# Kernel tuning notes

Hardware: AMD Instinct MI355X
Metric: run time of the kernel (lower is better)

## Reference

```python
import jax, jax.numpy as jnp
import numpy as np

N_NODES = 100000
NUM_REL = 2


def rgcn_conv(x, src, dst, etype, W, root, bias):
    """PyG-style RGCNConv: per-relation mean aggregation + root transform + bias.
    x: [N, in], W: [R, in, out], root: [in, out], bias: [out].
    """
    R = W.shape[0]
    N = x.shape[0]
    # Pre-transform nodes by every relation weight: [R, N, out]
    xr = jnp.einsum('ni,rio->rno', x, W)
    msgs = xr[etype, src]  # [E, out] gather per-edge, relation-typed
    seg_id = dst * R + etype  # combined (node, relation) segment id
    summed = jax.ops.segment_sum(msgs, seg_id, num_segments=N * R)
    cnt = jax.ops.segment_sum(jnp.ones(etype.shape, x.dtype), seg_id, num_segments=N * R)
    summed = summed.reshape(N, R, -1)
    cnt = cnt.reshape(N, R, 1)
    agg = (summed / jnp.maximum(cnt, 1.0)).sum(axis=1)  # sum over relations of per-relation means
    return agg + x @ root + bias


def setup_inputs() -> dict:
    key = jax.random.key(0)
    ks = jax.random.split(key, 9)
    d = 128
    E = 800000
    sc = 1.0 / np.sqrt(d)
    return {
        'x': jax.random.normal(ks[0], (N_NODES, d), jnp.float32),
        'edge_index_a': jax.random.randint(ks[1], (2, E), 0, N_NODES, jnp.int64),
        'edge_index_b': jax.random.randint(ks[2], (2, E), 0, N_NODES, jnp.int64),
        'W1': jax.random.normal(ks[3], (NUM_REL, d, d), jnp.float32) * sc,
        'root1': jax.random.normal(ks[4], (d, d), jnp.float32) * sc,
        'b1': jnp.zeros((d,), jnp.float32),
        'W2': jax.random.normal(ks[5], (NUM_REL, d, d), jnp.float32) * sc,
        'root2': jax.random.normal(ks[6], (d, d), jnp.float32) * sc,
        'b2': jnp.zeros((d,), jnp.float32),
    }


def reference(x, edge_index_a, edge_index_b, W1, root1, b1, W2, root2, b2):
    # Concatenate per-relation edge lists + build edge_type ids (a->0, b->1)
    edge_index = jnp.concatenate([edge_index_a, edge_index_b], axis=1)
    etype = jnp.concatenate([
        jnp.zeros((edge_index_a.shape[1],), jnp.int32),
        jnp.ones((edge_index_b.shape[1],), jnp.int32),
    ])
    src, dst = edge_index[0], edge_index[1]
    h = rgcn_conv(x, src, dst, etype, W1, root1, b1)
    h = jax.nn.relu(h)
    out = rgcn_conv(h, src, dst, etype, W2, root2, b2)
    return out
```

## Files before the change

kernel.cpp:

```cpp
#include <hip/hip_runtime.h>
#include <hip/hip_bf16.h>


typedef __attribute__((ext_vector_type(8))) short bf16x8;
typedef __attribute__((ext_vector_type(4))) float f32x4;
typedef unsigned short ushort_t;
typedef unsigned int uint_t;

#define BSHIFT 9
#define SEGB (1 << (BSHIFT + 1))
#define NBMAX 256
#define SLAB 16384
#define CH_PER_THREAD 8
#define CHUNK (256 * CH_PER_THREAD)

#define GBM 256
#define KCH 128
#define LDBE 136

#define ROWB 768
#define XOFF 512

__device__ __forceinline__ ushort_t f2b(float f) {
  union { float f; uint_t u; } v;
  v.f = f;
  uint_t u = v.u;
  return (ushort_t)((u + 0x7FFFu + ((u >> 16) & 1u)) >> 16);
}
__device__ __forceinline__ void dot2acc(float& a, uint_t pk, uint_t sel) {
  asm("v_dot2_f32_bf16 %0, %1, %2, %0" : "+v"(a) : "v"(pk), "v"(sel));
}

__global__ __launch_bounds__(256) void prep_bin(
    const int* __restrict__ ea, const int* __restrict__ eb, int E, int NB,
    int* __restrict__ cursor, uint_t* __restrict__ staging, int nchunk,
    const float* __restrict__ W1, const float* __restrict__ root1,
    const float* __restrict__ W2, const float* __restrict__ root2,
    ushort_t* __restrict__ Bt1, ushort_t* __restrict__ Bt2,
    const float* __restrict__ x, ushort_t* __restrict__ aggbuf1, int N) {
  __shared__ int h[NBMAX];
  __shared__ int bbase[NBMAX];
  __shared__ int lofs[NBMAX];
  __shared__ int sscan[256];
  __shared__ uint_t sval[CHUNK];
  __shared__ int sdst[CHUNK];
  int b = blockIdx.x;
  int t = threadIdx.x;

  if (b < nchunk) {
    for (int i = t; i < NB; i += 256) h[i] = 0;
    __syncthreads();
    int tbase = b * CHUNK + t;
    int total = 2 * E;
    uint_t val[CH_PER_THREAD];
    short bktv[CH_PER_THREAD];
#pragma unroll
    for (int j = 0; j < CH_PER_THREAD; ++j) {
      int i = tbase + j * 256;
      if (i < total) {
        int src, dst, rel;
        if (i < E) { src = ea[i];     dst = ea[E + i]; rel = 0; }
        else       { src = eb[i - E]; dst = eb[i];     rel = 1; }
        int seg = dst * 2 + rel;
        int bkt = seg >> (BSHIFT + 1);
        val[j] = ((uint_t)src << 10) | (uint_t)(seg & (SEGB - 1));
        bktv[j] = (short)bkt;
        atomicAdd(&h[bkt], 1);
      } else {
        bktv[j] = -1;
      }
    }
    __syncthreads();
    {
      int v = (t < NB) ? h[t] : 0;
      sscan[t] = v;
      __syncthreads();
      for (int off = 1; off < 256; off <<= 1) {
        int tmp = (t >= off) ? sscan[t - off] : 0;
        __syncthreads();
        sscan[t] += tmp;
        __syncthreads();
      }
      if (t < NB) {
        lofs[t] = sscan[t] - v;
        bbase[t] = v ? t * SLAB + atomicAdd(&cursor[t], v) : 0;
      }
    }
    __syncthreads();
    for (int i = t; i < NB; i += 256) h[i] = 0;
    __syncthreads();
#pragma unroll
    for (int j = 0; j < CH_PER_THREAD; ++j) {
      if (bktv[j] >= 0) {
        int bkt = bktv[j];
        int r = atomicAdd(&h[bkt], 1);
        int pos = lofs[bkt] + r;
        sval[pos] = val[j];
        sdst[pos] = bbase[bkt] + r;
      }
    }
    __syncthreads();
    int nrec = 2 * E - b * CHUNK;
    if (nrec > CHUNK) nrec = CHUNK;
    for (int i = t; i < nrec; i += 256)
      staging[sdst[i]] = sval[i];
  } else if (b < nchunk + 384) {
    int flat = (b - nchunk) * 256 + t;
    int which = flat >= 49152;
    int idx = flat - which * 49152;
    int c = idx / 384;
    int k = idx - c * 384;
    const float* W = which ? W2 : W1;
    const float* root = which ? root2 : root1;
    ushort_t* Bt = which ? Bt2 : Bt1;
    float v = (k < 256) ? W[(size_t)k * 128 + c] : root[(size_t)(k - 256) * 128 + c];
    Bt[(size_t)c * 384 + k] = f2b(v);
  } else {
    int idx = (b - nchunk - 384) * 256 + t;
    int n = idx >> 6, lane = idx & 63;
    if (n < N) {
      float2 v = *(const float2*)(x + (size_t)n * 128 + lane * 2);
      uint_t pk = (uint_t)f2b(v.x) | ((uint_t)f2b(v.y) << 16);
      *(uint_t*)(aggbuf1 + (size_t)n * 384 + 256 + lane * 2) = pk;
    }
  }
}

__global__ __launch_bounds__(1024) void bucket_build(
    const uint_t* __restrict__ staging, const int* __restrict__ cursor,
    int* __restrict__ csr, int* __restrict__ offs,
    int* __restrict__ ends, int nseg) {
  __shared__ int scnt[SEGB];
  __shared__ int sexcl[SEGB];
  __shared__ int sdata[SEGB];
  int b = blockIdx.x;
  int t = threadIdx.x;
  int base = b * SLAB;
  int ne = cursor[b];
  int seg0 = b << (BSHIFT + 1);

  scnt[t] = 0;
  __syncthreads();
  const uint_t* st = staging + base;
  for (int i = t; i < ne; i += 1024)
    atomicAdd(&scnt[st[i] & (SEGB - 1)], 1);
  __syncthreads();
  int c = scnt[t];
  sdata[t] = c;
  __syncthreads();
  for (int off = 1; off < 1024; off <<= 1) {
    int tmp = (t >= off) ? sdata[t - off] : 0;
    __syncthreads();
    sdata[t] += tmp;
    __syncthreads();
  }
  int excl = sdata[t] - c;
  sexcl[t] = excl;
  {
    int g = seg0 + t;
    if (g < nseg) { offs[g] = base + excl; ends[g] = base + excl + c; }
  }
  scnt[t] = 0;
  __syncthreads();
  for (int i = t; i < ne; i += 1024) {
    uint_t rec = st[i];
    int seg = (int)(rec & (SEGB - 1));
    int src = (int)(rec >> 10);
    int r = atomicAdd(&scnt[seg], 1);
    csr[base + sexcl[seg] + r] = src * ROWB + XOFF;
  }
}

__global__ __launch_bounds__(256) void agg_kernel(
    const char* __restrict__ xbc,
    const int* __restrict__ csr,
    const int* __restrict__ offs, const int* __restrict__ ends,
    ushort_t* __restrict__ agg, int nseg) {
  int wid = (blockIdx.x * blockDim.x + threadIdx.x) >> 6;
  if (wid >= nseg) return;
  int lane = threadIdx.x & 63;
  int q = lane >> 4;
  int t = lane & 15;
  int beg = offs[wid], end = ends[wid];
  const uint_t sel_lo = 0x00003F80u;
  const uint_t sel_hi = 0x3F800000u;

  float acc[8];
#pragma unroll
  for (int j = 0; j < 8; ++j) acc[j] = 0.f;

  const char* xt = xbc + t * 16;
  int e = beg + q;
  for (; e + 4 < end; e += 8) {
    int o0 = csr[e];
    int o1 = csr[e + 4];
    uint4 v0 = *(const uint4*)(xt + o0);
    uint4 v1 = *(const uint4*)(xt + o1);
    dot2acc(acc[0], v0.x, sel_lo); dot2acc(acc[1], v0.x, sel_hi);
    dot2acc(acc[2], v0.y, sel_lo); dot2acc(acc[3], v0.y, sel_hi);
    dot2acc(acc[4], v0.z, sel_lo); dot2acc(acc[5], v0.z, sel_hi);
    dot2acc(acc[6], v0.w, sel_lo); dot2acc(acc[7], v0.w, sel_hi);
    dot2acc(acc[0], v1.x, sel_lo); dot2acc(acc[1], v1.x, sel_hi);
    dot2acc(acc[2], v1.y, sel_lo); dot2acc(acc[3], v1.y, sel_hi);
    dot2acc(acc[4], v1.z, sel_lo); dot2acc(acc[5], v1.z, sel_hi);
    dot2acc(acc[6], v1.w, sel_lo); dot2acc(acc[7], v1.w, sel_hi);
  }
  if (e < end) {
    int o0 = csr[e];
    uint4 v0 = *(const uint4*)(xt + o0);
    dot2acc(acc[0], v0.x, sel_lo); dot2acc(acc[1], v0.x, sel_hi);
    dot2acc(acc[2], v0.y, sel_lo); dot2acc(acc[3], v0.y, sel_hi);
    dot2acc(acc[4], v0.z, sel_lo); dot2acc(acc[5], v0.z, sel_hi);
    dot2acc(acc[6], v0.w, sel_lo); dot2acc(acc[7], v0.w, sel_hi);
  }

#pragma unroll
  for (int j = 0; j < 8; ++j) {
    acc[j] += __shfl_xor(acc[j], 16);
    acc[j] += __shfl_xor(acc[j], 32);
  }

  int c = end - beg;
  float inv = 1.0f / (float)(c > 1 ? c : 1);
  if (q == 0) {
    uint4 o;
    o.x = (uint_t)f2b(acc[0] * inv) | ((uint_t)f2b(acc[1] * inv) << 16);
    o.y = (uint_t)f2b(acc[2] * inv) | ((uint_t)f2b(acc[3] * inv) << 16);
    o.z = (uint_t)f2b(acc[4] * inv) | ((uint_t)f2b(acc[5] * inv) << 16);
    o.w = (uint_t)f2b(acc[6] * inv) | ((uint_t)f2b(acc[7] * inv) << 16);
    int n = wid >> 1, r = wid & 1;
    *(uint4*)(agg + (size_t)n * 384 + r * 128 + t * 8) = o;
  }
}

__device__ __forceinline__ void do_mfma32(
    const char* bs, f32x4 (&acc)[4][8], const bf16x8 (&a)[4],
    int ks, int lrow, int kg) {
  bf16x8 b[8];
#pragma unroll
  for (int c = 0; c < 8; ++c)
    b[c] = *(const bf16x8*)(bs + (c * 16 + lrow) * (LDBE * 2) +
                            (ks * 4 + kg) * 16);
#pragma unroll
  for (int r = 0; r < 4; ++r)
#pragma unroll
    for (int c = 0; c < 8; ++c)
      acc[r][c] = __builtin_amdgcn_mfma_f32_16x16x32_bf16(a[r], b[c], acc[r][c], 0, 0, 0);
}

template <int MODE>
__global__ __launch_bounds__(256, 2) void mfma_gemm(
    const ushort_t* __restrict__ A,
    const ushort_t* __restrict__ Bt,
    const float* __restrict__ bias,
    float* __restrict__ outf,
    ushort_t* __restrict__ outb,
    int M) {
  __shared__ __align__(16) ushort_t Bs[2][128 * LDBE];
  const int tid = threadIdx.x;
  const int lane = tid & 63;
  const int wave = tid >> 6;
  const int lrow = lane & 15;
  const int kg = lane >> 4;
  const int rowbase = blockIdx.x * GBM + wave * 64;

  f32x4 acc[4][8];
#pragma unroll
  for (int r = 0; r < 4; ++r)
#pragma unroll
    for (int c = 0; c < 8; ++c) acc[r][c] = (f32x4){0.f, 0.f, 0.f, 0.f};

  uint4 stg[8];
#pragma unroll
  for (int j = 0; j < 8; ++j) {
    int flat = tid + j * 256;
    int col = flat >> 4;
    int q = flat & 15;
    stg[j] = *(const uint4*)(Bt + (size_t)col * 384 + q * 8);
  }
#pragma unroll
  for (int j = 0; j < 8; ++j) {
    int flat = tid + j * 256;
    int col = flat >> 4;
    int q = flat & 15;
    *(uint4*)((char*)&Bs[0][0] + col * (LDBE * 2) + q * 16) = stg[j];
  }
  __syncthreads();

  int cur = 0;
  for (int ch = 0; ch < 3; ++ch) {
    if (ch < 2) {
#pragma unroll
      for (int j = 0; j < 8; ++j) {
        int flat = tid + j * 256;
        int col = flat >> 4;
        int q = flat & 15;
        stg[j] = *(const uint4*)(Bt + (size_t)col * 384 + (ch + 1) * KCH + q * 8);
      }
    }
    const ushort_t* ab = A + (size_t)ch * KCH + kg * 8;
    const char* bsbase = (const char*)&Bs[0][0] + cur * (128 * LDBE * 2);
    bf16x8 aA[4], aB[4];
#pragma unroll
    for (int r = 0; r < 4; ++r)
      aA[r] = *(const bf16x8*)(ab + (size_t)(rowbase + r * 16 + lrow) * 384);
#pragma unroll
    for (int r = 0; r < 4; ++r)
      aB[r] = *(const bf16x8*)(ab + (size_t)(rowbase + r * 16 + lrow) * 384 + 32);
    do_mfma32(bsbase, acc, aA, 0, lrow, kg);
#pragma unroll
    for (int r = 0; r < 4; ++r)
      aA[r] = *(const bf16x8*)(ab + (size_t)(rowbase + r * 16 + lrow) * 384 + 64);
    do_mfma32(bsbase, acc, aB, 1, lrow, kg);
#pragma unroll
    for (int r = 0; r < 4; ++r)
      aB[r] = *(const bf16x8*)(ab + (size_t)(rowbase + r * 16 + lrow) * 384 + 96);
    do_mfma32(bsbase, acc, aA, 2, lrow, kg);
    do_mfma32(bsbase, acc, aB, 3, lrow, kg);
    if (ch < 2) {
#pragma unroll
      for (int j = 0; j < 8; ++j) {
        int flat = tid + j * 256;
        int col = flat >> 4;
        int q = flat & 15;
        *(uint4*)((char*)&Bs[0][0] + (cur ^ 1) * (128 * LDBE * 2) +
                  col * (LDBE * 2) + q * 16) = stg[j];
      }
      __syncthreads();
      cur ^= 1;
    }
  }

  if (MODE == 1) {
    __syncthreads();
    ushort_t* ws = (ushort_t*)&Bs[0][0] + wave * (64 * 128);
#pragma unroll
    for (int c = 0; c < 8; ++c) {
      int col = c * 16 + lrow;
      float bv = bias[col];
#pragma unroll
      for (int r = 0; r < 4; ++r)
#pragma unroll
        for (int j = 0; j < 4; ++j) {
          float v = fmaxf(acc[r][c][j] + bv, 0.f);
          ws[(r * 16 + kg * 4 + j) * 128 + col] = f2b(v);
        }
    }
    __syncthreads();
#pragma unroll
    for (int rr = 0; rr < 16; ++rr) {
      int lr = rr * 4 + (lane >> 4);
      int row = rowbase + lr;
      int tq = lane & 15;
      if (row < M) {
        uint4 v = *(const uint4*)(ws + lr * 128 + tq * 8);
        *(uint4*)(outb + (size_t)row * 384 + 256 + tq * 8) = v;
      }
    }
  } else {
#pragma unroll
    for (int c = 0; c < 8; ++c) {
      int col = c * 16 + lrow;
      float bv = bias[col];
#pragma unroll
      for (int r = 0; r < 4; ++r) {
        int r0 = rowbase + r * 16 + kg * 4;
#pragma unroll
        for (int j = 0; j < 4; ++j) {
          int row = r0 + j;
          if (row < M) {
            outf[(size_t)row * 128 + col] = acc[r][c][j] + bv;
          }
        }
      }
    }
  }
}

extern "C" void kernel_launch(void* const* d_in, const int* in_sizes, int n_in,
                              void* d_out, int out_size, void* d_ws, size_t ws_size,
                              hipStream_t stream) {
  const float* x     = (const float*)d_in[0];
  const int*   ea    = (const int*)d_in[1];
  const int*   eb    = (const int*)d_in[2];
  const float* W1    = (const float*)d_in[3];
  const float* root1 = (const float*)d_in[4];
  const float* b1    = (const float*)d_in[5];
  const float* W2    = (const float*)d_in[6];
  const float* root2 = (const float*)d_in[7];
  const float* b2    = (const float*)d_in[8];
  float* out = (float*)d_out;

  const int N = in_sizes[0] / 128;
  const int E = in_sizes[1] / 2;
  const int nseg = N * 2;
  const int Mblk = (N + GBM - 1) / GBM;
  const int Mpad = Mblk * GBM;
  const int NB = ((N - 1) >> BSHIFT) + 1;
  const int nchunk = (2 * E + CHUNK - 1) / CHUNK;
  const int XSB = (N * 64 + 255) / 256;

  char* p = (char*)d_ws;
  ushort_t* aggbuf1 = (ushort_t*)p;  p += (size_t)Mpad * 384 * sizeof(ushort_t);
  ushort_t* aggbuf2 = (ushort_t*)p;  p += (size_t)Mpad * 384 * sizeof(ushort_t);
  ushort_t* Bt1 = (ushort_t*)p;      p += (size_t)128 * 384 * sizeof(ushort_t);
  ushort_t* Bt2 = (ushort_t*)p;      p += (size_t)128 * 384 * sizeof(ushort_t);
  int* csr = (int*)p;                p += (size_t)NBMAX * SLAB * sizeof(int);
  int* offs = (int*)p;               p += (size_t)nseg * sizeof(int);
  int* ends = (int*)p;               p += (size_t)nseg * sizeof(int);
  int* cursor = (int*)p;             p += NBMAX * sizeof(int);
  uint_t* staging = (uint_t*)aggbuf2;

  hipMemsetAsync(cursor, 0, NBMAX * sizeof(int), stream);

  prep_bin<<<nchunk + 384 + XSB, 256, 0, stream>>>(
      ea, eb, E, NB, cursor, staging, nchunk,
      W1, root1, W2, root2, Bt1, Bt2, x, aggbuf1, N);

  bucket_build<<<NB, 1024, 0, stream>>>(staging, cursor, csr, offs, ends, nseg);

  const int agg_blocks = (nseg + 3) / 4;

  agg_kernel<<<agg_blocks, 256, 0, stream>>>((const char*)aggbuf1, csr, offs,
                                             ends, aggbuf1, nseg);
  mfma_gemm<1><<<Mblk, 256, 0, stream>>>(aggbuf1, Bt1, b1, nullptr, aggbuf2, N);

  agg_kernel<<<agg_blocks, 256, 0, stream>>>((const char*)aggbuf2, csr, offs,
                                             ends, aggbuf2, nseg);
  mfma_gemm<0><<<Mblk, 256, 0, stream>>>(aggbuf2, Bt2, b2, out, nullptr, N);
}
```

Before: 299.3 us.

## Shrink GEMM K-chunk to 96 for 3 blocks/CU, widen x conversion and agg unroll

The GEMM now stages B in 96-wide K chunks (LDS row stride 104) over four iterations instead of 128-wide over three. The shared-memory footprint drops, and the launch bound goes from 2 to 3 blocks per CU to raise occupancy. The bf16 epilogue is split into two 32-row passes so it fits the smaller LDS buffer. The x-to-bf16 conversion now handles 8 floats per thread with 16-byte stores, and the aggregation loop processes three edges per lane per iteration with a remainder loop. The trade-off is more chunk iterations and syncs, plus register pressure from forcing 3 blocks/CU with a 4x8 accumulator array, which may cause spills.

```diff
diff --git a/kernel.cpp b/kernel.cpp
--- a/kernel.cpp
+++ b/kernel.cpp
@@ -15,8 +15,8 @@
 #define CHUNK (256 * CH_PER_THREAD)
 
 #define GBM 256
-#define KCH 128
-#define LDBE 136
+#define KCH 96
+#define LDBE 104
 
 #define ROWB 768
 #define XOFF 512
@@ -117,11 +117,16 @@
     Bt[(size_t)c * 384 + k] = f2b(v);
   } else {
     int idx = (b - nchunk - 384) * 256 + t;
-    int n = idx >> 6, lane = idx & 63;
+    int n = idx >> 4, tq = idx & 15;
     if (n < N) {
-      float2 v = *(const float2*)(x + (size_t)n * 128 + lane * 2);
-      uint_t pk = (uint_t)f2b(v.x) | ((uint_t)f2b(v.y) << 16);
-      *(uint_t*)(aggbuf1 + (size_t)n * 384 + 256 + lane * 2) = pk;
+      float4 a = *(const float4*)(x + (size_t)n * 128 + tq * 8);
+      float4 c = *(const float4*)(x + (size_t)n * 128 + tq * 8 + 4);
+      uint4 o;
+      o.x = (uint_t)f2b(a.x) | ((uint_t)f2b(a.y) << 16);
+      o.y = (uint_t)f2b(a.z) | ((uint_t)f2b(a.w) << 16);
+      o.z = (uint_t)f2b(c.x) | ((uint_t)f2b(c.y) << 16);
+      o.w = (uint_t)f2b(c.z) | ((uint_t)f2b(c.w) << 16);
+      *(uint4*)(aggbuf1 + (size_t)n * 384 + 256 + tq * 8) = o;
     }
   }
 }
@@ -170,6 +175,12 @@
     csr[base + sexcl[seg] + r] = src * ROWB + XOFF;
   }
 }
+
+#define ACC8(v)                                               \
+  dot2acc(acc[0], v.x, sel_lo); dot2acc(acc[1], v.x, sel_hi); \
+  dot2acc(acc[2], v.y, sel_lo); dot2acc(acc[3], v.y, sel_hi); \
+  dot2acc(acc[4], v.z, sel_lo); dot2acc(acc[5], v.z, sel_hi); \
+  dot2acc(acc[6], v.w, sel_lo); dot2acc(acc[7], v.w, sel_hi);
 
 __global__ __launch_bounds__(256) void agg_kernel(
     const char* __restrict__ xbc,
@@ -191,27 +202,19 @@
 
   const char* xt = xbc + t * 16;
   int e = beg + q;
-  for (; e + 4 < end; e += 8) {
+  for (; e + 8 < end; e += 12) {
     int o0 = csr[e];
     int o1 = csr[e + 4];
+    int o2 = csr[e + 8];
     uint4 v0 = *(const uint4*)(xt + o0);
     uint4 v1 = *(const uint4*)(xt + o1);
-    dot2acc(acc[0], v0.x, sel_lo); dot2acc(acc[1], v0.x, sel_hi);
-    dot2acc(acc[2], v0.y, sel_lo); dot2acc(acc[3], v0.y, sel_hi);
-    dot2acc(acc[4], v0.z, sel_lo); dot2acc(acc[5], v0.z, sel_hi);
-    dot2acc(acc[6], v0.w, sel_lo); dot2acc(acc[7], v0.w, sel_hi);
-    dot2acc(acc[0], v1.x, sel_lo); dot2acc(acc[1], v1.x, sel_hi);
-    dot2acc(acc[2], v1.y, sel_lo); dot2acc(acc[3], v1.y, sel_hi);
-    dot2acc(acc[4], v1.z, sel_lo); dot2acc(acc[5], v1.z, sel_hi);
-    dot2acc(acc[6], v1.w, sel_lo); dot2acc(acc[7], v1.w, sel_hi);
-  }
-  if (e < end) {
+    uint4 v2 = *(const uint4*)(xt + o2);
+    ACC8(v0); ACC8(v1); ACC8(v2);
+  }
+  for (; e < end; e += 4) {
     int o0 = csr[e];
     uint4 v0 = *(const uint4*)(xt + o0);
-    dot2acc(acc[0], v0.x, sel_lo); dot2acc(acc[1], v0.x, sel_hi);
-    dot2acc(acc[2], v0.y, sel_lo); dot2acc(acc[3], v0.y, sel_hi);
-    dot2acc(acc[4], v0.z, sel_lo); dot2acc(acc[5], v0.z, sel_hi);
-    dot2acc(acc[6], v0.w, sel_lo); dot2acc(acc[7], v0.w, sel_hi);
+    ACC8(v0);
   }
 
 #pragma unroll
@@ -249,7 +252,7 @@
 }
 
 template <int MODE>
-__global__ __launch_bounds__(256, 2) void mfma_gemm(
+__global__ __launch_bounds__(256, 3) void mfma_gemm(
     const ushort_t* __restrict__ A,
     const ushort_t* __restrict__ Bt,
     const float* __restrict__ bias,
@@ -270,31 +273,31 @@
 #pragma unroll
     for (int c = 0; c < 8; ++c) acc[r][c] = (f32x4){0.f, 0.f, 0.f, 0.f};
 
-  uint4 stg[8];
-#pragma unroll
-  for (int j = 0; j < 8; ++j) {
+  uint4 stg[6];
+#pragma unroll
+  for (int j = 0; j < 6; ++j) {
     int flat = tid + j * 256;
-    int col = flat >> 4;
-    int q = flat & 15;
+    int col = flat / 12;
+    int q = flat - col * 12;
     stg[j] = *(const uint4*)(Bt + (size_t)col * 384 + q * 8);
   }
 #pragma unroll
-  for (int j = 0; j < 8; ++j) {
+  for (int j = 0; j < 6; ++j) {
     int flat = tid + j * 256;
-    int col = flat >> 4;
-    int q = flat & 15;
+    int col = flat / 12;
+    int q = flat - col * 12;
     *(uint4*)((char*)&Bs[0][0] + col * (LDBE * 2) + q * 16) = stg[j];
   }
   __syncthreads();
 
   int cur = 0;
-  for (int ch = 0; ch < 3; ++ch) {
-    if (ch < 2) {
-#pragma unroll
-      for (int j = 0; j < 8; ++j) {
+  for (int ch = 0; ch < 4; ++ch) {
+    if (ch < 3) {
+#pragma unroll
+      for (int j = 0; j < 6; ++j) {
         int flat = tid + j * 256;
-        int col = flat >> 4;
-        int q = flat & 15;
+        int col = flat / 12;
+        int q = flat - col * 12;
         stg[j] = *(const uint4*)(Bt + (size_t)col * 384 + (ch + 1) * KCH + q * 8);
       }
     }
@@ -312,17 +315,13 @@
     for (int r = 0; r < 4; ++r)
       aA[r] = *(const bf16x8*)(ab + (size_t)(rowbase + r * 16 + lrow) * 384 + 64);
     do_mfma32(bsbase, acc, aB, 1, lrow, kg);
-#pragma unroll
-    for (int r = 0; r < 4; ++r)
-      aB[r] = *(const bf16x8*)(ab + (size_t)(rowbase + r * 16 + lrow) * 384 + 96);
     do_mfma32(bsbase, acc, aA, 2, lrow, kg);
-    do_mfma32(bsbase, acc, aB, 3, lrow, kg);
-    if (ch < 2) {
-#pragma unroll
-      for (int j = 0; j < 8; ++j) {
+    if (ch < 3) {
+#pragma unroll
+      for (int j = 0; j < 6; ++j) {
         int flat = tid + j * 256;
-        int col = flat >> 4;
-        int q = flat & 15;
+        int col = flat / 12;
+        int q = flat - col * 12;
         *(uint4*)((char*)&Bs[0][0] + (cur ^ 1) * (128 * LDBE * 2) +
                   col * (LDBE * 2) + q * 16) = stg[j];
       }
@@ -332,29 +331,34 @@
   }
 
   if (MODE == 1) {
-    __syncthreads();
-    ushort_t* ws = (ushort_t*)&Bs[0][0] + wave * (64 * 128);
-#pragma unroll
-    for (int c = 0; c < 8; ++c) {
-      int col = c * 16 + lrow;
-      float bv = bias[col];
-#pragma unroll
-      for (int r = 0; r < 4; ++r)
-#pragma unroll
-        for (int j = 0; j < 4; ++j) {
-          float v = fmaxf(acc[r][c][j] + bv, 0.f);
-          ws[(r * 16 + kg * 4 + j) * 128 + col] = f2b(v);
+    ushort_t* ws = (ushort_t*)&Bs[0][0] + wave * (32 * 128);
+#pragma unroll
+    for (int p = 0; p < 2; ++p) {
+      __syncthreads();
+#pragma unroll
+      for (int c = 0; c < 8; ++c) {
+        int col = c * 16 + lrow;
+        float bv = bias[col];
+#pragma unroll
+        for (int r = 0; r < 2; ++r) {
+          int rr = p * 2 + r;
+#pragma unroll
+          for (int j = 0; j < 4; ++j) {
+            float v = fmaxf(acc[rr][c][j] + bv, 0.f);
+            ws[(r * 16 + kg * 4 + j) * 128 + col] = f2b(v);
+          }
         }
-    }
-    __syncthreads();
-#pragma unroll
-    for (int rr = 0; rr < 16; ++rr) {
-      int lr = rr * 4 + (lane >> 4);
-      int row = rowbase + lr;
-      int tq = lane & 15;
-      if (row < M) {
-        uint4 v = *(const uint4*)(ws + lr * 128 + tq * 8);
-        *(uint4*)(outb + (size_t)row * 384 + 256 + tq * 8) = v;
+      }
+      __syncthreads();
+#pragma unroll
+      for (int rr2 = 0; rr2 < 8; ++rr2) {
+        int lr = rr2 * 4 + (lane >> 4);
+        int row = rowbase + p * 32 + lr;
+        int tq = lane & 15;
+        if (row < M) {
+          uint4 v = *(const uint4*)(ws + lr * 128 + tq * 8);
+          *(uint4*)(outb + (size_t)row * 384 + 256 + tq * 8) = v;
+        }
       }
     }
   } else {
@@ -398,7 +402,7 @@
   const int Mpad = Mblk * GBM;
   const int NB = ((N - 1) >> BSHIFT) + 1;
   const int nchunk = (2 * E + CHUNK - 1) / CHUNK;
-  const int XSB = (N * 64 + 255) / 256;
+  const int XSB = (N * 16 + 255) / 256;
 
   char* p = (char*)d_ws;
   ushort_t* aggbuf1 = (ushort_t*)p;  p += (size_t)Mpad * 384 * sizeof(ushort_t);
```

Result: slower. 390.5 us (+30.4%).
